# Performance work log

Measured on AMD Instinct MI355X. Metric: run time of the kernel, lower is better.

## Reference

```python
import jax, jax.numpy as jnp
import numpy as np

S = 20  # amino-acid alphabet size (hardcoded in the layer)
EPS = 1e-16


def setup_inputs() -> dict:
    key = jax.random.key(0)
    k1, k2, k3, k4, k5 = jax.random.split(key, 5)
    m, b, L, k = 2, 256, 1024, 8
    return {
        "sequences": jax.random.uniform(k1, (m, b, L, S), dtype=jnp.float32),
        "exchangeability_kernel": jax.random.normal(k2, (m, k, S, S), dtype=jnp.float32),
        "equilibrium_kernel": jax.random.normal(k3, (m, k, S), dtype=jnp.float32),
        "tau_kernel": jax.random.normal(k4, (m, b), dtype=jnp.float32),
        "per_matrix_rates_kernel": jax.random.normal(k5, (m, k), dtype=jnp.float32),
    }


def _anc_probs(sequences, exch_kernel, eq_kernel, tau_kernel, pmr_kernel):
    eye = jnp.eye(S, dtype=sequences.dtype)
    # make_R: symmetrize, softplus, zero diagonal -> exchangeabilities (m,k,s,s)
    K = 0.5 * (exch_kernel + jnp.swapaxes(exch_kernel, -1, -2))
    R = jax.nn.softplus(K) * (1.0 - eye)
    # make_p: equilibrium distribution via softmax (m,k,s)
    p = jax.nn.softmax(eq_kernel, axis=-1)
    # make_rate_matrix: Q_ij = R_ij * p_j, diag = -rowsum, normalize to 1 sub/site
    Q = R * p[..., None, :]
    row = jnp.sum(Q, axis=-1)                      # (m,k,s)
    Q = Q - row[..., None] * eye
    mue = jnp.sum(p * row, axis=-1)                # (m,k) expected rate
    Q = Q / jnp.maximum(mue, EPS)[..., None, None]
    # branch lengths: softplus, per-matrix rates: softplus -> tau (m,b,k)
    tau = jax.nn.softplus(tau_kernel)              # (m,b)
    rho = jax.nn.softplus(pmr_kernel)              # (m,k)
    tau_mbk = tau[:, :, None] * rho[:, None, :]    # (m,b,k)
    # GTR expm via symmetrization: S_sym = D^{1/2} Q D^{-1/2} (symmetric)
    sp = jnp.sqrt(p)                               # (m,k,s)
    isp = 1.0 / sp
    Ssym = sp[..., :, None] * Q * isp[..., None, :]
    Ssym = 0.5 * (Ssym + jnp.swapaxes(Ssym, -1, -2))
    lam, U = jnp.linalg.eigh(Ssym)                 # (m,k,s), (m,k,s,s)
    E = jnp.exp(tau_mbk[..., None] * lam[:, None, :, :])  # (m,b,k,s)
    # P = D^{-1/2} U exp(tau*Lam) U^T D^{1/2}  -> (m,b,k,s,s)
    P = jnp.einsum('mkie,mbke,mkje->mbkij', U, E, U)
    P = isp[:, None, :, :, None] * P * sp[:, None, :, None, :]
    # prob lookup for vector-format sequences (not transposed)
    return jnp.einsum('mblz,mbkzs->mblks', sequences, P)


def reference(sequences, exchangeability_kernel, equilibrium_kernel, tau_kernel, per_matrix_rates_kernel):
    return _anc_probs(sequences, exchangeability_kernel, equilibrium_kernel,
                      tau_kernel, per_matrix_rates_kernel)
```

## Files before the change

kernel.cpp:

```cpp
#include <hip/hip_runtime.h>

#define AS 20
#define ASS 400
#define KK 8
#define BB 256
#define MM 2
#define LL 1024
#define NPOW 12

typedef __attribute__((ext_vector_type(8))) short bf16x8;
typedef __attribute__((ext_vector_type(16))) float f32x16;

__device__ __forceinline__ unsigned short f2bf(float x) {
    unsigned int u = __builtin_bit_cast(unsigned int, x);
    u += 0x7FFFu + ((u >> 16) & 1u);
    return (unsigned short)(u >> 16);
}

__device__ __forceinline__ float softplus_f(float x) {
    return x > 20.f ? x : log1pf(expf(x));
}

__device__ __forceinline__ void wsync() {
    __builtin_amdgcn_sched_barrier(0);
    asm volatile("s_waitcnt lgkmcnt(0)" ::: "memory");
    __builtin_amdgcn_sched_barrier(0);
}

__device__ __forceinline__ void mul20w(const float* __restrict__ A,
                                       const float* __restrict__ B,
                                       float* __restrict__ C, int lane) {
    wsync();
    if (lane < 50) {
        const int i2 = (lane / 5) * 2;
        const int c4 = (lane % 5) * 4;
        float a0[AS], a1[AS];
        #pragma unroll
        for (int q = 0; q < 5; q++) {
            float4 v0 = *(const float4*)&A[i2 * AS + 4 * q];
            float4 v1 = *(const float4*)&A[(i2 + 1) * AS + 4 * q];
            a0[4*q] = v0.x; a0[4*q+1] = v0.y; a0[4*q+2] = v0.z; a0[4*q+3] = v0.w;
            a1[4*q] = v1.x; a1[4*q+1] = v1.y; a1[4*q+2] = v1.z; a1[4*q+3] = v1.w;
        }
        float4 s0 = {0.f,0.f,0.f,0.f}, s1 = {0.f,0.f,0.f,0.f};
        #pragma unroll
        for (int z = 0; z < AS; z++) {
            float4 bv = *(const float4*)&B[z * AS + c4];
            s0.x = fmaf(a0[z], bv.x, s0.x); s0.y = fmaf(a0[z], bv.y, s0.y);
            s0.z = fmaf(a0[z], bv.z, s0.z); s0.w = fmaf(a0[z], bv.w, s0.w);
            s1.x = fmaf(a1[z], bv.x, s1.x); s1.y = fmaf(a1[z], bv.y, s1.y);
            s1.z = fmaf(a1[z], bv.z, s1.z); s1.w = fmaf(a1[z], bv.w, s1.w);
        }
        *(float4*)&C[i2 * AS + c4] = s0;
        *(float4*)&C[(i2 + 1) * AS + c4] = s1;
    }
}

__global__ __launch_bounds__(256) void prep_powers_par(
    const float* __restrict__ exch, const float* __restrict__ eqk,
    const float* __restrict__ pmr,
    float* __restrict__ Spow_g,
    float* __restrict__ sp_g, float* __restrict__ isp_g,
    float* __restrict__ rho_g, float* __restrict__ nrm_g)
{
    const int mk = blockIdx.x;
    const int t = threadIdx.x;
    const int w = t >> 6, lane = t & 63;
    __shared__ float p[AS], sp[AS], isp[AS], rowsum[AS], rowabs[AS];
    __shared__ __align__(16) float SL[NPOW * ASS];

    const float* Km = exch + (size_t)mk * ASS;
    const float* ev = eqk + (size_t)mk * AS;

    if (t < AS) {
        float mx = -1e30f;
        for (int i = 0; i < AS; i++) mx = fmaxf(mx, ev[i]);
        float sum = 0.f;
        for (int i = 0; i < AS; i++) sum += expf(ev[i] - mx);
        float pl = expf(ev[t] - mx) / sum;
        p[t] = pl;
        float sq = sqrtf(pl);
        sp[t] = sq; isp[t] = 1.0f / sq;
    }
    if (t == 0) rho_g[mk] = softplus_f(pmr[mk]);
    __syncthreads();

    float* RP   = SL + ASS;
    float* RawS = SL + 2 * ASS;
    for (int f = t; f < ASS; f += 256) {
        int i = f / AS, j = f % AS;
        float Kv = 0.5f * (Km[i*AS+j] + Km[j*AS+i]);
        float Rv = (i == j) ? 0.f : softplus_f(Kv);
        RP[f] = Rv * p[j];
    }
    __syncthreads();
    if (t < AS) {
        float r = 0.f;
        for (int j = 0; j < AS; j++) r += RP[t*AS+j];
        rowsum[t] = r;
    }
    __syncthreads();
    float mue = 0.f;
    for (int i = 0; i < AS; i++) mue += p[i] * rowsum[i];
    const float inv_mue = 1.0f / fmaxf(mue, 1e-16f);
    for (int f = t; f < ASS; f += 256) {
        int i = f / AS, j = f % AS;
        float Qv = (RP[f] - (i == j ? rowsum[i] : 0.f)) * inv_mue;
        RawS[f] = sp[i] * Qv * isp[j];
    }
    __syncthreads();
    for (int f = t; f < ASS; f += 256) {
        int i = f / AS, j = f % AS;
        SL[f] = 0.5f * (RawS[f] + RawS[j*AS+i]);
    }
    __syncthreads();
    if (t < AS) {
        float r = 0.f;
        for (int j = 0; j < AS; j++) r += fabsf(SL[t*AS+j]);
        rowabs[t] = r;
    }
    __syncthreads();
    if (t == 0) {
        float n = 0.f;
        for (int i = 0; i < AS; i++) n = fmaxf(n, rowabs[i]);
        nrm_g[mk] = n;
    }
    if (t < AS) { sp_g[mk*AS + t] = sp[t]; isp_g[mk*AS + t] = isp[t]; }

    if (w == 0) mul20w(SL, SL, SL + ASS, lane);
    __syncthreads();
    if (w == 0) mul20w(SL + ASS, SL,       SL + 2*ASS, lane);
    if (w == 1) mul20w(SL + ASS, SL + ASS, SL + 3*ASS, lane);
    __syncthreads();
    if (w == 0) mul20w(SL + 3*ASS, SL,         SL + 4*ASS, lane);
    if (w == 1) mul20w(SL + 3*ASS, SL + ASS,   SL + 5*ASS, lane);
    if (w == 2) mul20w(SL + 3*ASS, SL + 2*ASS, SL + 6*ASS, lane);
    if (w == 3) mul20w(SL + 3*ASS, SL + 3*ASS, SL + 7*ASS, lane);
    __syncthreads();
    if (w == 0) mul20w(SL + 7*ASS, SL,         SL + 8*ASS, lane);
    if (w == 1) mul20w(SL + 7*ASS, SL + ASS,   SL + 9*ASS, lane);
    if (w == 2) mul20w(SL + 7*ASS, SL + 2*ASS, SL + 10*ASS, lane);
    if (w == 3) mul20w(SL + 7*ASS, SL + 3*ASS, SL + 11*ASS, lane);
    __syncthreads();

    float* Sg = Spow_g + (size_t)mk * NPOW * ASS;
    for (int f = t; f < NPOW * ASS; f += 256) Sg[f] = SL[f];
}

__global__ __launch_bounds__(320, 4) void fused_apply(
    const float* __restrict__ seq, const float* __restrict__ Spow_g,
    const float* __restrict__ sp_g, const float* __restrict__ isp_g,
    const float* __restrict__ rho_g, const float* __restrict__ nrm_g,
    const float* __restrict__ tauk, float* __restrict__ out)
{
    const int blk = blockIdx.x;
    const int mb = blk >> 1;
    const int half = blk & 1;
    const int mi = mb / BB;
    const int t = threadIdx.x;
    const int w = t >> 6;
    const int lane = t & 63;

    __shared__ __align__(16) float regionA[KK * ASS];
    __shared__ __align__(16) float Tmp[5 * ASS];
    __shared__ float coefs[KK][NPOW];
    __shared__ float spk[KK * AS], ispk[KK * AS];
    __shared__ float scs[KK];
    __shared__ int ssh[KK];

    float* Plds = regionA;

    const int rowbase = half * (LL / 2);
    const float* seqb = seq + (size_t)mb * LL * AS;
    float* outb = out + (size_t)mb * LL * (KK * AS);

    const float4 first = ((const float4*)(seqb + (size_t)rowbase * AS))[t];

    if (t < KK) {
        const float tau = softplus_f(tauk[mb]) * rho_g[mi * KK + t];
        const float nt = tau * nrm_g[mi * KK + t];
        int s = 0;
        if (nt > 2.0f) {
            s = (int)ceilf(log2f(nt * 0.5f));
            if (s < 0) s = 0;
            if (s > 12) s = 12;
        }
        ssh[t] = s;
        scs[t] = ldexpf(tau, -s);
    }
    if (t < KK * AS) {
        spk[t]  = sp_g [mi * KK * AS + t];
        ispk[t] = isp_g[mi * KK * AS + t];
    }
    __syncthreads();
    if (t < KK * NPOW) {
        const int k = t / NPOW, n = t % NPOW + 1;
        const float sc = scs[k];
        float scp = sc, fact = 1.f;
        for (int q = 2; q <= n; ++q) { scp *= sc; fact *= (float)q; }
        coefs[k][n - 1] = scp / fact;
    }
    __syncthreads();

    {
        const float* Sbase = Spow_g + (size_t)mi * KK * NPOW * ASS;
        #pragma unroll 2
        for (int e = t; e < KK * ASS; e += 320) {
            const int k = e / ASS;
            const int f = e - k * ASS;
            const int i = f / AS, jj = f - i * AS;
            const float* Sg = Sbase + (size_t)k * NPOW * ASS + f;
            float acc = (i == jj) ? 1.f : 0.f;
            #pragma unroll
            for (int n = 1; n <= NPOW; ++n)
                acc = fmaf(coefs[k][n - 1], Sg[(n - 1) * ASS], acc);
            Plds[e] = acc;
        }
    }
    __syncthreads();

    {
        const int nk = (w < 3) ? 2 : 1;
        for (int pi = 0; pi < nk; ++pi) {
            const int k = (pi == 0) ? w : w + 5;
            const int s = ssh[k];
            float* Pk = &Plds[k * ASS];
            float* Tw = &Tmp[w * ASS];
            for (int q = 0; q < s; ++q) {
                if ((q & 1) == 0) mul20w(Pk, Pk, Tw, lane);
                else              mul20w(Tw, Tw, Pk, lane);
            }
            if (s & 1) {
                wsync();
                if (lane < 50) {
                    #pragma unroll
                    for (int u = 0; u < 8; ++u) Pk[lane * 8 + u] = Tw[lane * 8 + u];
                }
            }
        }
    }
    __syncthreads();

    for (int e = t; e < KK * ASS; e += 320) {
        const int k = e / ASS;
        const int f = e - k * ASS;
        const int i = f / AS, jj = f - i * AS;
        Plds[e] *= ispk[k * AS + i] * spk[k * AS + jj];
    }
    __syncthreads();

    const int mycol = w * 32 + (lane & 31);
    const int bki = mycol / 20, bs = mycol % 20;
    const float* Pcol = Plds + bki * ASS + bs;
    bf16x8 bf0, bf1;
    #pragma unroll
    for (int jj = 0; jj < 8; ++jj) {
        const int k0 = (lane >> 5) * 8 + jj;
        const int k1 = 16 + k0;
        bf0[jj] = (short)f2bf(Pcol[k0 * AS]);
        bf1[jj] = (k1 < AS) ? (short)f2bf(Pcol[k1 * AS]) : (short)0;
    }
    __syncthreads();

    unsigned short* tile = (unsigned short*)regionA;
    for (int i = t; i < 384; i += 320) {
        const int b = i / 192, r = (i % 192) / 3, q = i % 3;
        *(uint2*)((char*)tile + b * 5120 + r * 80 + 40 + q * 8) = make_uint2(0u, 0u);
    }
    {
        const int r = t / 5, pc = t % 5;
        const unsigned int lo = (unsigned)f2bf(first.x) | ((unsigned)f2bf(first.y) << 16);
        const unsigned int hi = (unsigned)f2bf(first.z) | ((unsigned)f2bf(first.w) << 16);
        *(uint2*)((char*)tile + r * 80 + pc * 8) = make_uint2(lo, hi);
    }
    __syncthreads();

    for (int c = 0; c < 8; ++c) {
        const int cur = c & 1;
        float4 rnext;
        if (c < 7)
            rnext = ((const float4*)(seqb + (size_t)(rowbase + (c + 1) * 64) * AS))[t];

        const char* tb = (const char*)tile + cur * 5120;
        float* chout = outb + (size_t)(rowbase + c * 64) * 160;

        #pragma unroll
        for (int tr = 0; tr < 2; ++tr) {
            const char* arow = tb + (tr * 32 + (lane & 31)) * 80 + (lane >> 5) * 16;
            const bf16x8 a0 = *(const bf16x8*)(arow);
            const bf16x8 a1 = *(const bf16x8*)(arow + 32);
            f32x16 d = {0.f,0.f,0.f,0.f,0.f,0.f,0.f,0.f,
                        0.f,0.f,0.f,0.f,0.f,0.f,0.f,0.f};
            d = __builtin_amdgcn_mfma_f32_32x32x16_bf16(a0, bf0, d, 0, 0, 0);
            d = __builtin_amdgcn_mfma_f32_32x32x16_bf16(a1, bf1, d, 0, 0, 0);
            float* sb = chout + (size_t)(tr * 32 + (lane >> 5) * 4) * 160
                        + w * 32 + (lane & 31);
            #pragma unroll
            for (int r = 0; r < 16; ++r) {
                const int rl = (r & 3) + 8 * (r >> 2);
                __builtin_nontemporal_store(d[r], sb + rl * 160);
            }
        }

        if (c < 7) {
            const int r = t / 5, pc = t % 5;
            const unsigned int lo = (unsigned)f2bf(rnext.x) | ((unsigned)f2bf(rnext.y) << 16);
            const unsigned int hi = (unsigned)f2bf(rnext.z) | ((unsigned)f2bf(rnext.w) << 16);
            *(uint2*)((char*)tile + (cur ^ 1) * 5120 + r * 80 + pc * 8) = make_uint2(lo, hi);
        }
        __syncthreads();
    }
}

extern "C" void kernel_launch(void* const* d_in, const int* in_sizes, int n_in,
                              void* d_out, int out_size, void* d_ws, size_t ws_size,
                              hipStream_t stream) {
    const float* seq  = (const float*)d_in[0];
    const float* exch = (const float*)d_in[1];
    const float* eqk  = (const float*)d_in[2];
    const float* tauk = (const float*)d_in[3];
    const float* pmr  = (const float*)d_in[4];
    float* out = (float*)d_out;

    float* ws   = (float*)d_ws;
    float* Spow = ws;
    float* spg  = Spow + (size_t)MM * KK * NPOW * ASS;
    float* ispg = spg + MM * KK * AS;
    float* rhog = ispg + MM * KK * AS;
    float* nrmg = rhog + MM * KK;

    prep_powers_par<<<dim3(MM * KK), dim3(256), 0, stream>>>(
        exch, eqk, pmr, Spow, spg, ispg, rhog, nrmg);
    fused_apply<<<dim3(MM * BB * 2), dim3(320), 0, stream>>>(
        seq, Spow, spg, ispg, rhog, nrmg, tauk, out);
}
```

Measured before the change: 85.61 us.

## Give each wave its own row range and all five column tiles

The block shrinks from 5 waves to 4. Each wave now owns 128 rows of the half-sequence and computes all five 32-column output tiles itself, holding five B fragments in registers. Each wave stages its rows in a private LDS tile, which removes the per-chunk block-wide barriers, and it issues all of its global loads up front. The cost is more LDS (about 40KB for the tile region) and more registers, with the occupancy target lowered to 3 blocks per CU.

```diff
diff --git a/kernel.cpp b/kernel.cpp
--- a/kernel.cpp
+++ b/kernel.cpp
@@ -147,7 +147,7 @@
     for (int f = t; f < NPOW * ASS; f += 256) Sg[f] = SL[f];
 }
 
-__global__ __launch_bounds__(320, 4) void fused_apply(
+__global__ __launch_bounds__(256, 3) void fused_apply(
     const float* __restrict__ seq, const float* __restrict__ Spow_g,
     const float* __restrict__ sp_g, const float* __restrict__ isp_g,
     const float* __restrict__ rho_g, const float* __restrict__ nrm_g,
@@ -161,8 +161,8 @@
     const int w = t >> 6;
     const int lane = t & 63;
 
-    __shared__ __align__(16) float regionA[KK * ASS];
-    __shared__ __align__(16) float Tmp[5 * ASS];
+    __shared__ __align__(16) float regionA[10240];
+    __shared__ __align__(16) float Tmp[4 * ASS];
     __shared__ float coefs[KK][NPOW];
     __shared__ float spk[KK * AS], ispk[KK * AS];
     __shared__ float scs[KK];
@@ -170,11 +170,16 @@
 
     float* Plds = regionA;
 
-    const int rowbase = half * (LL / 2);
+    const int rowstart0 = half * (LL / 2) + w * 128;
     const float* seqb = seq + (size_t)mb * LL * AS;
     float* outb = out + (size_t)mb * LL * (KK * AS);
 
-    const float4 first = ((const float4*)(seqb + (size_t)rowbase * AS))[t];
+    float4 sA[5];
+    {
+        const float4* g0 = (const float4*)(seqb + (size_t)rowstart0 * AS);
+        #pragma unroll
+        for (int u = 0; u < 5; ++u) sA[u] = g0[lane + 64 * u];
+    }
 
     if (t < KK) {
         const float tau = softplus_f(tauk[mb]) * rho_g[mi * KK + t];
@@ -204,8 +209,7 @@
 
     {
         const float* Sbase = Spow_g + (size_t)mi * KK * NPOW * ASS;
-        #pragma unroll 2
-        for (int e = t; e < KK * ASS; e += 320) {
+        for (int e = t; e < KK * ASS; e += 256) {
             const int k = e / ASS;
             const int f = e - k * ASS;
             const int i = f / AS, jj = f - i * AS;
@@ -220,9 +224,9 @@
     __syncthreads();
 
     {
-        const int nk = (w < 3) ? 2 : 1;
-        for (int pi = 0; pi < nk; ++pi) {
-            const int k = (pi == 0) ? w : w + 5;
+        #pragma unroll
+        for (int pi = 0; pi < 2; ++pi) {
+            const int k = w + pi * 4;
             const int s = ssh[k];
             float* Pk = &Plds[k * ASS];
             float* Tw = &Tmp[w * ASS];
@@ -241,7 +245,7 @@
     }
     __syncthreads();
 
-    for (int e = t; e < KK * ASS; e += 320) {
+    for (int e = t; e < KK * ASS; e += 256) {
         const int k = e / ASS;
         const int f = e - k * ASS;
         const int i = f / AS, jj = f - i * AS;
@@ -249,67 +253,83 @@
     }
     __syncthreads();
 
-    const int mycol = w * 32 + (lane & 31);
-    const int bki = mycol / 20, bs = mycol % 20;
-    const float* Pcol = Plds + bki * ASS + bs;
-    bf16x8 bf0, bf1;
+    bf16x8 bf0[5], bf1[5];
     #pragma unroll
-    for (int jj = 0; jj < 8; ++jj) {
-        const int k0 = (lane >> 5) * 8 + jj;
-        const int k1 = 16 + k0;
-        bf0[jj] = (short)f2bf(Pcol[k0 * AS]);
-        bf1[jj] = (k1 < AS) ? (short)f2bf(Pcol[k1 * AS]) : (short)0;
-    }
-    __syncthreads();
-
-    unsigned short* tile = (unsigned short*)regionA;
-    for (int i = t; i < 384; i += 320) {
-        const int b = i / 192, r = (i % 192) / 3, q = i % 3;
-        *(uint2*)((char*)tile + b * 5120 + r * 80 + 40 + q * 8) = make_uint2(0u, 0u);
-    }
+    for (int ct = 0; ct < 5; ++ct) {
+        const int mycol = ct * 32 + (lane & 31);
+        const int bki = mycol / 20, bs = mycol % 20;
+        const float* Pcol = Plds + bki * ASS + bs;
+        #pragma unroll
+        for (int jj = 0; jj < 8; ++jj) {
+            const int k0 = (lane >> 5) * 8 + jj;
+            const int k1 = 16 + k0;
+            bf0[ct][jj] = (short)f2bf(Pcol[k0 * AS]);
+            bf1[ct][jj] = (k1 < AS) ? (short)f2bf(Pcol[k1 * AS]) : (short)0;
+        }
+    }
+    __syncthreads();
+
+    char* mytile = (char*)regionA + w * 10240;
+
+    for (int i = lane; i < 640; i += 64) {
+        const int b = i / 320, rem = i % 320, r = rem / 5, q = rem % 5;
+        *(uint2*)(mytile + b * 5120 + r * 80 + 40 + q * 8) = make_uint2(0u, 0u);
+    }
+
+    #define PACK_CHUNK(SRC, BUFOFF)                                              \
+        {                                                                        \
+            _Pragma("unroll")                                                    \
+            for (int u = 0; u < 5; ++u) {                                        \
+                const int t5 = lane + 64 * u;                                    \
+                const int r = t5 / 5, pc = t5 % 5;                               \
+                const unsigned int lo = (unsigned)f2bf(SRC[u].x)                 \
+                                      | ((unsigned)f2bf(SRC[u].y) << 16);        \
+                const unsigned int hi = (unsigned)f2bf(SRC[u].z)                 \
+                                      | ((unsigned)f2bf(SRC[u].w) << 16);        \
+                *(uint2*)(mytile + (BUFOFF) + r * 80 + pc * 8) = make_uint2(lo, hi); \
+            }                                                                    \
+        }
+
+    #define COMPUTE_CHUNK(BUFOFF, ROWSTART)                                      \
+        {                                                                        \
+            wsync();                                                             \
+            _Pragma("unroll")                                                    \
+            for (int tr = 0; tr < 2; ++tr) {                                     \
+                const char* arow = mytile + (BUFOFF)                             \
+                                 + (tr * 32 + (lane & 31)) * 80 + (lane >> 5) * 16; \
+                const bf16x8 a0 = *(const bf16x8*)(arow);                        \
+                const bf16x8 a1 = *(const bf16x8*)(arow + 32);                   \
+                _Pragma("unroll")                                                \
+                for (int ct = 0; ct < 5; ++ct) {                                 \
+                    f32x16 d = {0.f,0.f,0.f,0.f,0.f,0.f,0.f,0.f,                 \
+                                0.f,0.f,0.f,0.f,0.f,0.f,0.f,0.f};                \
+                    d = __builtin_amdgcn_mfma_f32_32x32x16_bf16(a0, bf0[ct], d, 0, 0, 0); \
+                    d = __builtin_amdgcn_mfma_f32_32x32x16_bf16(a1, bf1[ct], d, 0, 0, 0); \
+                    float* sb = outb + (size_t)((ROWSTART) + tr * 32             \
+                                + (lane >> 5) * 4) * 160 + ct * 32 + (lane & 31); \
+                    _Pragma("unroll")                                            \
+                    for (int r = 0; r < 16; ++r) {                               \
+                        const int rl = (r & 3) + 8 * (r >> 2);                   \
+                        __builtin_nontemporal_store(d[r], sb + rl * 160);        \
+                    }                                                            \
+                }                                                                \
+            }                                                                    \
+        }
+
+    PACK_CHUNK(sA, 0)
+    float4 sB[5];
     {
-        const int r = t / 5, pc = t % 5;
-        const unsigned int lo = (unsigned)f2bf(first.x) | ((unsigned)f2bf(first.y) << 16);
-        const unsigned int hi = (unsigned)f2bf(first.z) | ((unsigned)f2bf(first.w) << 16);
-        *(uint2*)((char*)tile + r * 80 + pc * 8) = make_uint2(lo, hi);
-    }
-    __syncthreads();
-
-    for (int c = 0; c < 8; ++c) {
-        const int cur = c & 1;
-        float4 rnext;
-        if (c < 7)
-            rnext = ((const float4*)(seqb + (size_t)(rowbase + (c + 1) * 64) * AS))[t];
-
-        const char* tb = (const char*)tile + cur * 5120;
-        float* chout = outb + (size_t)(rowbase + c * 64) * 160;
-
-        #pragma unroll
-        for (int tr = 0; tr < 2; ++tr) {
-            const char* arow = tb + (tr * 32 + (lane & 31)) * 80 + (lane >> 5) * 16;
-            const bf16x8 a0 = *(const bf16x8*)(arow);
-            const bf16x8 a1 = *(const bf16x8*)(arow + 32);
-            f32x16 d = {0.f,0.f,0.f,0.f,0.f,0.f,0.f,0.f,
-                        0.f,0.f,0.f,0.f,0.f,0.f,0.f,0.f};
-            d = __builtin_amdgcn_mfma_f32_32x32x16_bf16(a0, bf0, d, 0, 0, 0);
-            d = __builtin_amdgcn_mfma_f32_32x32x16_bf16(a1, bf1, d, 0, 0, 0);
-            float* sb = chout + (size_t)(tr * 32 + (lane >> 5) * 4) * 160
-                        + w * 32 + (lane & 31);
-            #pragma unroll
-            for (int r = 0; r < 16; ++r) {
-                const int rl = (r & 3) + 8 * (r >> 2);
-                __builtin_nontemporal_store(d[r], sb + rl * 160);
-            }
-        }
-
-        if (c < 7) {
-            const int r = t / 5, pc = t % 5;
-            const unsigned int lo = (unsigned)f2bf(rnext.x) | ((unsigned)f2bf(rnext.y) << 16);
-            const unsigned int hi = (unsigned)f2bf(rnext.z) | ((unsigned)f2bf(rnext.w) << 16);
-            *(uint2*)((char*)tile + (cur ^ 1) * 5120 + r * 80 + pc * 8) = make_uint2(lo, hi);
-        }
-        __syncthreads();
-    }
+        const float4* g1 = (const float4*)(seqb + (size_t)(rowstart0 + 64) * AS);
+        #pragma unroll
+        for (int u = 0; u < 5; ++u) sB[u] = g1[lane + 64 * u];
+    }
+
+    PACK_CHUNK(sB, 5120)
+    COMPUTE_CHUNK(0, rowstart0)
+    COMPUTE_CHUNK(5120, rowstart0 + 64)
+
+    #undef PACK_CHUNK
+    #undef COMPUTE_CHUNK
 }
 
 extern "C" void kernel_launch(void* const* d_in, const int* in_sizes, int n_in,
@@ -331,6 +351,6 @@
 
     prep_powers_par<<<dim3(MM * KK), dim3(256), 0, stream>>>(
         exch, eqk, pmr, Spow, spg, ispg, rhog, nrmg);
-    fused_apply<<<dim3(MM * BB * 2), dim3(320), 0, stream>>>(
+    fused_apply<<<dim3(MM * BB * 2), dim3(256), 0, stream>>>(
         seq, Spow, spg, ispg, rhog, nrmg, tauk, out);
 }
```

After: 90.30 us. +5.5%, slower.
